# Kernel tuning notes

Hardware: AMD Instinct MI355X
Metric: run time of the kernel (lower is better)

The kernel has to match this reference:

```python
import jax, jax.numpy as jnp
import numpy as np

B, NV, NC, D, GD = 4, 2048, 8192, 64, 8


def setup_inputs() -> dict:
    key = jax.random.key(0)
    ks = jax.random.split(key, 16)
    f32 = jnp.float32
    rn = lambda k, s, fan: (jax.random.normal(k, s, dtype=f32) / np.float32(np.sqrt(fan)))
    raw = jax.random.randint(ks[0], (B, NC, NV), 0, 20)
    c_mat = jnp.where(raw == 0, -1.0, jnp.where(raw == 1, 1.0, 0.0)).astype(f32)
    v_mat = jnp.transpose(c_mat, (0, 2, 1))  # [B, NV, NC]
    variables = jax.random.normal(ks[1], (B, NV, D), dtype=f32)
    ground_vars = jax.random.normal(ks[2], (B, NV, GD), dtype=f32)
    # learned params
    c_block = rn(ks[3], (2, D, D), D)  # pos/neg literal projections (clause side)
    v_block = rn(ks[4], (2, D, D), D)  # pos/neg literal projections (variable side)
    vb = jax.random.normal(ks[5], (D,), dtype=f32)
    cb = jax.random.normal(ks[6], (D,), dtype=f32)
    Wg = rn(ks[7], (D, GD + D), GD + D)  # ground combiner Linear(concat) -> D
    bg = jnp.zeros((D,), f32)
    Wz = rn(ks[8], (D, D), D); Uz = rn(ks[9], (D, D), D); bz = jnp.zeros((D,), f32)
    Wr = rn(ks[10], (D, D), D); Ur = rn(ks[11], (D, D), D); br = jnp.zeros((D,), f32)
    Wh = rn(ks[12], (D, D), D); Uh = rn(ks[13], (D, D), D); bh = jnp.zeros((D,), f32)
    return dict(variables=variables, ground_vars=ground_vars, c_mat=c_mat, v_mat=v_mat,
                c_block=c_block, v_block=v_block, vb=vb, cb=cb, Wg=Wg, bg=bg,
                Wz=Wz, Uz=Uz, bz=bz, Wr=Wr, Ur=Ur, br=br, Wh=Wh, Uh=Uh, bh=bh)


def reference(variables, ground_vars, c_mat, v_mat, c_block, v_block, vb, cb,
              Wg, bg, Wz, Uz, bz, Wr, Ur, br, Wh, Uh, bh):
    b, nv, d = variables.shape
    v = variables.reshape(-1, d)  # [B*NV, D]
    # clause-side literal projections: bmm(c_block, v^T)^T == v @ c_block[i]^T
    pos_vars = (v @ c_block[0].T).reshape(b, nv, d)
    neg_vars = (v @ c_block[1].T).reshape(b, nv, d)
    pos_cmat = jnp.clip(c_mat, 0.0, 1.0)
    neg_cmat = -jnp.clip(c_mat, -1.0, 0.0)
    c = (jnp.einsum('bcv,bvd->bcd', pos_cmat, pos_vars)
         + jnp.einsum('bcv,bvd->bcd', neg_cmat, neg_vars))  # [B, NC, D]
    c = jax.nn.relu(c + cb)
    cv = c.reshape(-1, d)  # [B*NC, D]
    pos_cvars = (cv @ v_block[0].T).reshape(b, -1, d)
    neg_cvars = (cv @ v_block[1].T).reshape(b, -1, d)
    pos_vmat = jnp.clip(v_mat, 0.0, 1.0)
    neg_vmat = -jnp.clip(v_mat, -1.0, 0.0)
    nv_msg = (jnp.einsum('bvc,bcd->bvd', pos_vmat, pos_cvars)
              + jnp.einsum('bvc,bcd->bvd', neg_vmat, neg_cvars))  # [B, NV, D]
    v_emb = jax.nn.relu(nv_msg + vb).reshape(-1, d)
    # ground combiner: tanh(Linear(concat(ground, v_emb)))
    g = ground_vars.reshape(-1, ground_vars.shape[-1])
    av = jnp.tanh(jnp.concatenate([g, v_emb], axis=-1) @ Wg.T + bg)
    # GRU update against previous variable embeddings
    prev = v
    z = jax.nn.sigmoid(av @ Wz.T + prev @ Uz.T + bz)
    r = jax.nn.sigmoid(av @ Wr.T + prev @ Ur.T + br)
    h_tilda = jnp.tanh(av @ Wh.T + (r * prev) @ Uh.T + bh)
    h = (1.0 - z) * prev + z * h_tilda
    return h.reshape(b, nv * d, 1)
```

## Files before the change

### kernel.cpp

```cpp
#include <hip/hip_runtime.h>
#include <hip/hip_bf16.h>
#include <stdint.h>

#define NBATCH 4
#define NV 2048
#define NC 8192
#define DD 64

typedef __attribute__((ext_vector_type(8))) short s16x8;
typedef __attribute__((ext_vector_type(4))) float fx4;
typedef __attribute__((ext_vector_type(8))) unsigned short u16x8;
typedef __attribute__((ext_vector_type(4))) int i32x4;
typedef __attribute__((ext_vector_type(2))) unsigned int u32x2;

static __device__ __forceinline__ void gload_lds16(const void* g, void* l) {
    __builtin_amdgcn_global_load_lds(
        (const __attribute__((address_space(1))) unsigned int*)g,
        (__attribute__((address_space(3))) unsigned int*)l, 16, 0, 0);
}

__global__ __launch_bounds__(256) void k_prep_pv(
    const float* __restrict__ vars, const float* __restrict__ cblk,
    char* __restrict__ qsh, char* __restrict__ qsl,
    char* __restrict__ qdh, char* __restrict__ qdl)
{
    __shared__ float sv[32][64];
    __shared__ float scb[2][64][65];
    int blk = blockIdx.x;
    int b = blk >> 6, ch = blk & 63;
    int t = threadIdx.x;
    const float* vsrc = vars + ((size_t)b * NV + (size_t)ch * 32) * DD;
    for (int i = t; i < 32 * 64; i += 256) sv[i >> 6][i & 63] = vsrc[i];
    for (int i = t; i < 2 * 64 * 64; i += 256) {
        int pn = i >> 12, dout = (i >> 6) & 63, k = i & 63;
        scb[pn][k][dout] = cblk[i];
    }
    __syncthreads();
    int ks = t >> 6, dout = t & 63;
    unsigned int wsh[2] = {0, 0}, wsl[2] = {0, 0}, wdh[2] = {0, 0}, wdl[2] = {0, 0};
    #pragma unroll
    for (int c8 = 0; c8 < 8; ++c8) {
        int vloc = ks * 8 + c8;
        float ap = 0.f, an = 0.f;
        for (int k = 0; k < 64; ++k) {
            float vv = sv[vloc][k];
            ap += vv * scb[0][k][dout];
            an += vv * scb[1][k][dout];
        }
        float s = (ap + an) * 0.5f, dv = (ap - an) * 0.5f;
        int qs_ = (int)rintf(s * 4096.f);
        int qd_ = (int)rintf(dv * 4096.f);
        qs_ = min(max(qs_, -32511), 32511);
        qd_ = min(max(qd_, -32511), 32511);
        int sh = (qs_ + 128) >> 8, sl = qs_ - (sh << 8);
        int dh = (qd_ + 128) >> 8, dl = qd_ - (dh << 8);
        int w = c8 >> 2, sft = (c8 & 3) * 8;
        wsh[w] |= (unsigned int)(sh & 0xFF) << sft;
        wsl[w] |= (unsigned int)(sl & 0xFF) << sft;
        wdh[w] |= (unsigned int)(dh & 0xFF) << sft;
        wdl[w] |= (unsigned int)(dl & 0xFF) << sft;
    }
    int kc = ch >> 1;
    int lg = ((ch & 1) << 1) | (ks >> 1);
    size_t off = (((size_t)(b * 32 + kc) * 64 + dout) * 4 + lg) * 16 + (ks & 1) * 8;
    *(u32x2*)(qsh + off) = (u32x2){wsh[0], wsh[1]};
    *(u32x2*)(qsl + off) = (u32x2){wsl[0], wsl[1]};
    *(u32x2*)(qdh + off) = (u32x2){wdh[0], wdh[1]};
    *(u32x2*)(qdl + off) = (u32x2){wdl[0], wdl[1]};
}

__global__ __launch_bounds__(256) void k_compress(
    const float* __restrict__ cmat,
    char* __restrict__ asgn, unsigned short* __restrict__ comp)
{
    __shared__ char sb[64][272];
    int blk = blockIdx.x;
    int tv = blk & 7;
    int rg = (blk >> 3) & 127;
    int b = blk >> 10;
    int t = threadIdx.x;
    int wv = t >> 6, l = t & 63;
    int crow0 = rg * 64;
    const float* src = cmat + (size_t)b * NC * NV + (size_t)crow0 * NV + tv * 256;
    #pragma unroll 4
    for (int rr = 0; rr < 16; ++rr) {
        int r = wv * 16 + rr;
        fx4 x = *(const fx4*)(src + (size_t)r * NV + l * 4);
        unsigned int pk = ((unsigned int)((int)x[0] & 0xFF))
                        | (((unsigned int)((int)x[1] & 0xFF)) << 8)
                        | (((unsigned int)((int)x[2] & 0xFF)) << 16)
                        | (((unsigned int)((int)x[3] & 0xFF)) << 24);
        *(unsigned int*)&sb[r][l * 4] = pk;
    }
    __syncthreads();
    size_t abase = ((size_t)(b * 128 + tv * 16)) * 8192 * 16;
    #pragma unroll
    for (int ff = 0; ff < 4; ++ff) {
        int f = wv * 4 + ff;
        i32x4 v = *(const i32x4*)&sb[l][f * 16];
        *(i32x4*)(asgn + abase + ((size_t)f * 8192 + crow0 + l) * 16) = v;
    }
    unsigned short* cbp = comp + ((size_t)b * 256 + tv * 32) * NC + crow0;
    #pragma unroll
    for (int it = 0; it < 8; ++it) {
        int idx = it * 256 + t;
        int v8l = idx >> 6, r = idx & 63;
        const unsigned char* p = (const unsigned char*)&sb[r][v8l * 8];
        unsigned int c0 = 0;
        #pragma unroll
        for (int i = 0; i < 8; ++i) c0 |= ((unsigned int)(p[i] & 3u)) << (2 * i);
        cbp[(size_t)v8l * NC + r] = (unsigned short)c0;
    }
}

__global__ __launch_bounds__(256, 4) void k_phaseA(
    const char* __restrict__ asgn,
    const char* __restrict__ qsh, const char* __restrict__ qsl,
    const char* __restrict__ qdh, const char* __restrict__ qdl,
    float* __restrict__ cpart)
{
    __shared__ char lds[2][16384];
    int blk = blockIdx.x;
    int combo = blk & 15;
    int rg = blk >> 4;
    int b = combo >> 2;
    int q = combo & 3;
    int t = threadIdx.x;
    int wv = t >> 6, l = t & 63, lr = l & 15, lg = l >> 4;
    int c0 = rg * 128 + wv * 32;

    i32x4 ahi[2][4], alo[2][4];
    #pragma unroll
    for (int i = 0; i < 2; ++i)
        #pragma unroll
        for (int j = 0; j < 4; ++j) { ahi[i][j] = (i32x4){0,0,0,0}; alo[i][j] = (i32x4){0,0,0,0}; }

    {
        size_t gb = ((size_t)(b * 32 + q * 8)) * 4096 + (size_t)t * 16;
        char* lp = &lds[0][t * 16];
        gload_lds16(qsh + gb, lp);
        gload_lds16(qsl + gb, lp + 4096);
        gload_lds16(qdh + gb, lp + 8192);
        gload_lds16(qdl + gb, lp + 12288);
    }
    __syncthreads();

    int cur = 0;
    #pragma unroll 1
    for (int cc = 0; cc < 8; ++cc) {
        int kc = q * 8 + cc;
        if (cc < 7) {
            size_t gb = ((size_t)(b * 32 + kc + 1)) * 4096 + (size_t)t * 16;
            char* lp = &lds[cur ^ 1][t * 16];
            gload_lds16(qsh + gb, lp);
            gload_lds16(qsl + gb, lp + 4096);
            gload_lds16(qdh + gb, lp + 8192);
            gload_lds16(qdl + gb, lp + 12288);
        }
        i32x4 Asgn[2], Aabs[2];
        #pragma unroll
        for (int rt = 0; rt < 2; ++rt) {
            size_t ao = (((size_t)(b * 128 + kc * 4 + lg)) * 8192
                         + (size_t)(c0 + rt * 16 + lr)) * 16;
            i32x4 sg = *(const i32x4*)(asgn + ao);
            Asgn[rt] = sg;
            i32x4 ab;
            #pragma unroll
            for (int w = 0; w < 4; ++w) ab[w] = sg[w] & 0x01010101;
            Aabs[rt] = ab;
        }
        const char* bufp = lds[cur];
        #pragma unroll
        for (int n = 0; n < 4; ++n) {
            int boff = ((n * 16 + lr) * 4 + lg) * 16;
            i32x4 Bsh = *(const i32x4*)(bufp + boff);
            i32x4 Bsl = *(const i32x4*)(bufp + 4096 + boff);
            i32x4 Bdh = *(const i32x4*)(bufp + 8192 + boff);
            i32x4 Bdl = *(const i32x4*)(bufp + 12288 + boff);
            #pragma unroll
            for (int rt = 0; rt < 2; ++rt) {
                ahi[rt][n] = __builtin_amdgcn_mfma_i32_16x16x64_i8(Aabs[rt], Bsh, ahi[rt][n], 0, 0, 0);
                ahi[rt][n] = __builtin_amdgcn_mfma_i32_16x16x64_i8(Asgn[rt], Bdh, ahi[rt][n], 0, 0, 0);
                alo[rt][n] = __builtin_amdgcn_mfma_i32_16x16x64_i8(Aabs[rt], Bsl, alo[rt][n], 0, 0, 0);
                alo[rt][n] = __builtin_amdgcn_mfma_i32_16x16x64_i8(Asgn[rt], Bdl, alo[rt][n], 0, 0, 0);
            }
        }
        __syncthreads();
        cur ^= 1;
    }
    float* dst = cpart + (((size_t)q * NBATCH + b) * NC + c0) * DD;
    #pragma unroll
    for (int rt = 0; rt < 2; ++rt)
        #pragma unroll
        for (int n = 0; n < 4; ++n)
            #pragma unroll
            for (int r = 0; r < 4; ++r) {
                float v = (float)(ahi[rt][n][r] * 256 + alo[rt][n][r]) * (1.0f / 4096.0f);
                dst[(size_t)(rt * 16 + lg * 4 + r) * DD + n * 16 + lr] = v;
            }
}

__global__ __launch_bounds__(256) void k_projC(
    const float* __restrict__ cpart, const float* __restrict__ cb,
    const float* __restrict__ vblk,
    char* __restrict__ csh, char* __restrict__ csl,
    char* __restrict__ cdh, char* __restrict__ cdl)
{
    __shared__ float src[32][64];
    __shared__ float svb[2][64][65];
    int blk = blockIdx.x;
    int b = blk >> 8, kc32 = blk & 255;
    int t = threadIdx.x;
    const size_t qs = (size_t)NBATCH * NC * DD;
    const float* cs = cpart + ((size_t)b * NC + (size_t)kc32 * 32) * DD;
    for (int i = t; i < 2048; i += 256) {
        int k = i & 63;
        float v = cb[k];
        #pragma unroll
        for (int p = 0; p < 4; ++p) v += cs[i + p * qs];
        src[i >> 6][k] = fmaxf(v, 0.f);
    }
    for (int i = t; i < 8192; i += 256) {
        int pn = i >> 12, dout = (i >> 6) & 63, k = i & 63;
        svb[pn][k][dout] = vblk[i];
    }
    __syncthreads();
    int ks = t >> 6, dout = t & 63;
    float ap[8] = {0.f, 0.f, 0.f, 0.f, 0.f, 0.f, 0.f, 0.f};
    float an[8] = {0.f, 0.f, 0.f, 0.f, 0.f, 0.f, 0.f, 0.f};
    for (int k = 0; k < 64; ++k) {
        float w0 = svb[0][k][dout], w1 = svb[1][k][dout];
        #pragma unroll
        for (int c8 = 0; c8 < 8; ++c8) {
            float rc = src[ks * 8 + c8][k];
            ap[c8] += rc * w0;
            an[c8] += rc * w1;
        }
    }
    unsigned int wsh[2] = {0, 0}, wsl[2] = {0, 0}, wdh[2] = {0, 0}, wdl[2] = {0, 0};
    #pragma unroll
    for (int c8 = 0; c8 < 8; ++c8) {
        float s = (ap[c8] + an[c8]) * 0.5f, dv = (ap[c8] - an[c8]) * 0.5f;
        int q_s = (int)rintf(s * 512.f);
        int q_d = (int)rintf(dv * 512.f);
        q_s = min(max(q_s, -32511), 32511);
        q_d = min(max(q_d, -32511), 32511);
        int sh = (q_s + 128) >> 8, sl = q_s - (sh << 8);
        int dh = (q_d + 128) >> 8, dl = q_d - (dh << 8);
        int w = c8 >> 2, sft = (c8 & 3) * 8;
        wsh[w] |= (unsigned int)(sh & 0xFF) << sft;
        wsl[w] |= (unsigned int)(sl & 0xFF) << sft;
        wdh[w] |= (unsigned int)(dh & 0xFF) << sft;
        wdl[w] |= (unsigned int)(dl & 0xFF) << sft;
    }
    int kc = kc32 >> 1;
    int lgw = ((kc32 & 1) << 1) | (ks >> 1);
    size_t off = (((size_t)(b * 128 + kc) * 64 + dout) * 4 + lgw) * 16 + (ks & 1) * 8;
    *(u32x2*)(csh + off) = (u32x2){wsh[0], wsh[1]};
    *(u32x2*)(csl + off) = (u32x2){wsl[0], wsl[1]};
    *(u32x2*)(cdh + off) = (u32x2){wdh[0], wdh[1]};
    *(u32x2*)(cdl + off) = (u32x2){wdl[0], wdl[1]};
}

__global__ __launch_bounds__(256, 4) void k_phaseB(
    const unsigned short* __restrict__ comp,
    const char* __restrict__ csh, const char* __restrict__ csl,
    const char* __restrict__ cdh, const char* __restrict__ cdl,
    float* __restrict__ npart)
{
    __shared__ char lds[2][16384];
    int blk = blockIdx.x;
    int combo = blk & 63;
    int rg = blk >> 6;
    int b = combo >> 4;
    int q = combo & 15;
    int t = threadIdx.x;
    int wv = t >> 6, l = t & 63, lr = l & 15, lg = l >> 4;
    int v0 = rg * 128 + wv * 32;
    const unsigned short* compb = comp + (size_t)b * 256 * NC;
    int sh_ = 2 * (lr & 7);
    const unsigned short* cp0 = compb + (size_t)((v0 + lr) >> 3) * NC + q * 512 + lg * 16;
    const unsigned short* cp1 = compb + (size_t)((v0 + 16 + lr) >> 3) * NC + q * 512 + lg * 16;
    const size_t cbase = ((size_t)(b * 128 + q * 8)) * 4096;

    i32x4 ahi[2][4], alo[2][4];
    #pragma unroll
    for (int i = 0; i < 2; ++i)
        #pragma unroll
        for (int j = 0; j < 4; ++j) { ahi[i][j] = (i32x4){0,0,0,0}; alo[i][j] = (i32x4){0,0,0,0}; }

    {
        size_t gb = cbase + (size_t)t * 16;
        char* lp = &lds[0][t * 16];
        gload_lds16(csh + gb, lp);
        gload_lds16(csl + gb, lp + 4096);
        gload_lds16(cdh + gb, lp + 8192);
        gload_lds16(cdl + gb, lp + 12288);
    }
    __syncthreads();

    int cur = 0;
    #pragma unroll 1
    for (int cc = 0; cc < 8; ++cc) {
        u16x8 u00 = *(const u16x8*)(cp0 + cc * 64);
        u16x8 u01 = *(const u16x8*)(cp0 + cc * 64 + 8);
        u16x8 u10 = *(const u16x8*)(cp1 + cc * 64);
        u16x8 u11 = *(const u16x8*)(cp1 + cc * 64 + 8);
        if (cc < 7) {
            size_t gb = cbase + (size_t)(cc + 1) * 4096 + (size_t)t * 16;
            char* lp = &lds[cur ^ 1][t * 16];
            gload_lds16(csh + gb, lp);
            gload_lds16(csl + gb, lp + 4096);
            gload_lds16(cdh + gb, lp + 8192);
            gload_lds16(cdl + gb, lp + 12288);
        }
        i32x4 Asgn[2], Aabs[2];
        #pragma unroll
        for (int rt = 0; rt < 2; ++rt) {
            u16x8 ua = rt ? u10 : u00;
            u16x8 ub = rt ? u11 : u01;
            i32x4 sg;
            #pragma unroll
            for (int g = 0; g < 4; ++g) {
                unsigned int wg = 0;
                #pragma unroll
                for (int jj = 0; jj < 4; ++jj) {
                    int j = g * 4 + jj;
                    unsigned int code = ((unsigned int)(j < 8 ? ua[j & 7] : ub[j & 7]) >> sh_) & 3u;
                    unsigned int byt = (code == 3u) ? 0xFFu : code;
                    wg |= byt << (jj * 8);
                }
                sg[g] = (int)wg;
            }
            Asgn[rt] = sg;
            i32x4 ab;
            #pragma unroll
            for (int g = 0; g < 4; ++g) ab[g] = sg[g] & 0x01010101;
            Aabs[rt] = ab;
        }
        const char* bufp = lds[cur];
        #pragma unroll
        for (int n = 0; n < 4; ++n) {
            int boff = ((n * 16 + lr) * 4 + lg) * 16;
            i32x4 Bsh = *(const i32x4*)(bufp + boff);
            i32x4 Bsl = *(const i32x4*)(bufp + 4096 + boff);
            i32x4 Bdh = *(const i32x4*)(bufp + 8192 + boff);
            i32x4 Bdl = *(const i32x4*)(bufp + 12288 + boff);
            #pragma unroll
            for (int rt = 0; rt < 2; ++rt) {
                ahi[rt][n] = __builtin_amdgcn_mfma_i32_16x16x64_i8(Aabs[rt], Bsh, ahi[rt][n], 0, 0, 0);
                ahi[rt][n] = __builtin_amdgcn_mfma_i32_16x16x64_i8(Asgn[rt], Bdh, ahi[rt][n], 0, 0, 0);
                alo[rt][n] = __builtin_amdgcn_mfma_i32_16x16x64_i8(Aabs[rt], Bsl, alo[rt][n], 0, 0, 0);
                alo[rt][n] = __builtin_amdgcn_mfma_i32_16x16x64_i8(Asgn[rt], Bdl, alo[rt][n], 0, 0, 0);
            }
        }
        __syncthreads();
        cur ^= 1;
    }
    float* dst = npart + (((size_t)q * NBATCH + b) * NV + v0) * DD;
    #pragma unroll
    for (int rt = 0; rt < 2; ++rt)
        #pragma unroll
        for (int n = 0; n < 4; ++n)
            #pragma unroll
            for (int r = 0; r < 4; ++r) {
                float v = (float)(ahi[rt][n][r] * 256 + alo[rt][n][r]) * (1.0f / 512.0f);
                dst[(size_t)(rt * 16 + lg * 4 + r) * DD + n * 16 + lr] = v;
            }
}

__global__ __launch_bounds__(512) void k_gru(
    const float* __restrict__ npart, const float* __restrict__ vars,
    const float* __restrict__ gv, const float* __restrict__ vb,
    const float* __restrict__ Wg, const float* __restrict__ bg,
    const float* __restrict__ Wz, const float* __restrict__ Uz, const float* __restrict__ bz,
    const float* __restrict__ Wr, const float* __restrict__ Ur, const float* __restrict__ brr,
    const float* __restrict__ Wh, const float* __restrict__ Uh, const float* __restrict__ bh,
    float* __restrict__ out)
{
    __shared__ float sWg[72][65];
    __shared__ float sWz[64][65], sUz[64][65];
    __shared__ float sWr[64][65], sUr[64][65];
    __shared__ float sWh[64][65], sUh[64][65];
    __shared__ float scat[8][72];
    __shared__ float sprev[8][64];
    __shared__ float sav[8][64];
    __shared__ float srp[8][64];
    int t = threadIdx.x;
    for (int i = t * 4; i < 4608; i += 2048) {
        fx4 g4 = *(const fx4*)(Wg + i);
        int dout = i / 72, j = i - dout * 72;
        #pragma unroll
        for (int jj = 0; jj < 4; ++jj) sWg[j + jj][dout] = g4[jj];
    }
    for (int i = t * 4; i < 4096; i += 2048) {
        int dout = i >> 6, k = i & 63;
        fx4 a;
        a = *(const fx4*)(Wz + i);
        #pragma unroll
        for (int jj = 0; jj < 4; ++jj) sWz[k + jj][dout] = a[jj];
        a = *(const fx4*)(Uz + i);
        #pragma unroll
        for (int jj = 0; jj < 4; ++jj) sUz[k + jj][dout] = a[jj];
        a = *(const fx4*)(Wr + i);
        #pragma unroll
        for (int jj = 0; jj < 4; ++jj) sWr[k + jj][dout] = a[jj];
        a = *(const fx4*)(Ur + i);
        #pragma unroll
        for (int jj = 0; jj < 4; ++jj) sUr[k + jj][dout] = a[jj];
        a = *(const fx4*)(Wh + i);
        #pragma unroll
        for (int jj = 0; jj < 4; ++jj) sWh[k + jj][dout] = a[jj];
        a = *(const fx4*)(Uh + i);
        #pragma unroll
        for (int jj = 0; jj < 4; ++jj) sUh[k + jj][dout] = a[jj];
    }
    int rr = t >> 6, dout = t & 63;
    const size_t qs = (size_t)NBATCH * NV * DD;
    #pragma unroll 1
    for (int it = 0; it < 4; ++it) {
        size_t row = (size_t)blockIdx.x * 32 + it * 8 + rr;
        float prev = vars[row * 64 + dout];
        float ve = vb[dout];
        #pragma unroll
        for (int s = 0; s < 16; ++s) ve += npart[(size_t)s * qs + row * 64 + dout];
        ve = fmaxf(ve, 0.f);
        scat[rr][8 + dout] = ve;
        if (dout < 8) scat[rr][dout] = gv[row * 8 + dout];
        sprev[rr][dout] = prev;
        __syncthreads();
        float a = bg[dout];
        for (int j = 0; j < 72; ++j) a += scat[rr][j] * sWg[j][dout];
        float av = 1.f - 2.f / (__expf(2.f * a) + 1.f);
        sav[rr][dout] = av;
        __syncthreads();
        float zi = bz[dout], ri = brr[dout], hwa = 0.f;
        for (int k = 0; k < 64; ++k) {
            float ak = sav[rr][k], pk = sprev[rr][k];
            zi += ak * sWz[k][dout] + pk * sUz[k][dout];
            ri += ak * sWr[k][dout] + pk * sUr[k][dout];
            hwa += ak * sWh[k][dout];
        }
        float z = 1.f / (1.f + __expf(-zi));
        float rgate = 1.f / (1.f + __expf(-ri));
        srp[rr][dout] = rgate * prev;
        __syncthreads();
        float hin = bh[dout] + hwa;
        for (int k = 0; k < 64; ++k) hin += srp[rr][k] * sUh[k][dout];
        float ht = 1.f - 2.f / (__expf(2.f * hin) + 1.f);
        out[row * 64 + dout] = (1.f - z) * prev + z * ht;
        __syncthreads();
    }
}

extern "C" void kernel_launch(void* const* d_in, const int* in_sizes, int n_in,
                              void* d_out, int out_size, void* d_ws, size_t ws_size,
                              hipStream_t stream) {
    (void)in_sizes; (void)n_in; (void)out_size; (void)ws_size;
    const float* vars = (const float*)d_in[0];
    const float* gv   = (const float*)d_in[1];
    const float* cmat = (const float*)d_in[2];
    const float* cblk = (const float*)d_in[4];
    const float* vblk = (const float*)d_in[5];
    const float* vb   = (const float*)d_in[6];
    const float* cb   = (const float*)d_in[7];
    const float* Wg   = (const float*)d_in[8];
    const float* bg   = (const float*)d_in[9];
    const float* Wz   = (const float*)d_in[10];
    const float* Uz   = (const float*)d_in[11];
    const float* bz   = (const float*)d_in[12];
    const float* Wr   = (const float*)d_in[13];
    const float* Ur   = (const float*)d_in[14];
    const float* br_  = (const float*)d_in[15];
    const float* Wh   = (const float*)d_in[16];
    const float* Uh   = (const float*)d_in[17];
    const float* bh   = (const float*)d_in[18];
    float* out = (float*)d_out;

    char* w = (char*)d_ws;
    const size_t MB = 1024 * 1024;
    char* qsh = w + 0 * MB;
    char* qsl = w + 1 * MB;
    char* qdh = w + 2 * MB;
    char* qdl = w + 3 * MB;
    char* csh = w + 4 * MB;
    char* csl = w + 6 * MB;
    char* cdh = w + 8 * MB;
    char* cdl = w + 10 * MB;
    float* cpart         = (float*)(w + 12 * MB);
    float* npart         = (float*)(w + 44 * MB);
    unsigned short* comp = (unsigned short*)(w + 76 * MB);
    char* asgn           = w + 92 * MB;

    k_prep_pv<<<256, 256, 0, stream>>>(vars, cblk, qsh, qsl, qdh, qdl);
    k_compress<<<4096, 256, 0, stream>>>(cmat, asgn, comp);
    k_phaseA<<<1024, 256, 0, stream>>>(asgn, qsh, qsl, qdh, qdl, cpart);
    k_projC<<<1024, 256, 0, stream>>>(cpart, cb, vblk, csh, csl, cdh, cdl);
    k_phaseB<<<1024, 256, 0, stream>>>(comp, csh, csl, cdh, cdl, npart);
    k_gru<<<256, 512, 0, stream>>>(npart, vars, gv, vb, Wg, bg,
                                   Wz, Uz, bz, Wr, Ur, br_, Wh, Uh, bh, out);
}
```

Measured before the change: 186.3 us.

## Drop int8 sign matrix; decode 2-bit compressed adjacency inside phaseA

The compress kernel no longer writes a separate int8 signed adjacency array (64 MB total). Phase A instead reads the existing 2-bit packed `comp` array and expands it to int8 MFMA operands in registers, prefetching the next chunk's words one iteration ahead. This removes a large global write and read in exchange for extra ALU bit-unpacking in the MFMA loop and narrow 16-bit strided loads. The compress kernel also reads LDS with word loads instead of byte loads and shrinks its padding.

New measurement: 164.3 us. -11.8%, faster.

```diff
diff --git a/kernel.cpp b/kernel.cpp
--- a/kernel.cpp
+++ b/kernel.cpp
@@ -70,10 +70,9 @@
 }
 
 __global__ __launch_bounds__(256) void k_compress(
-    const float* __restrict__ cmat,
-    char* __restrict__ asgn, unsigned short* __restrict__ comp)
+    const float* __restrict__ cmat, unsigned short* __restrict__ comp)
 {
-    __shared__ char sb[64][272];
+    __shared__ char sb[64][260];
     int blk = blockIdx.x;
     int tv = blk & 7;
     int rg = (blk >> 3) & 127;
@@ -93,28 +92,24 @@
         *(unsigned int*)&sb[r][l * 4] = pk;
     }
     __syncthreads();
-    size_t abase = ((size_t)(b * 128 + tv * 16)) * 8192 * 16;
-    #pragma unroll
-    for (int ff = 0; ff < 4; ++ff) {
-        int f = wv * 4 + ff;
-        i32x4 v = *(const i32x4*)&sb[l][f * 16];
-        *(i32x4*)(asgn + abase + ((size_t)f * 8192 + crow0 + l) * 16) = v;
-    }
     unsigned short* cbp = comp + ((size_t)b * 256 + tv * 32) * NC + crow0;
     #pragma unroll
     for (int it = 0; it < 8; ++it) {
         int idx = it * 256 + t;
         int v8l = idx >> 6, r = idx & 63;
-        const unsigned char* p = (const unsigned char*)&sb[r][v8l * 8];
+        unsigned int lo = *(const unsigned int*)&sb[r][v8l * 8];
+        unsigned int hi = *(const unsigned int*)&sb[r][v8l * 8 + 4];
         unsigned int c0 = 0;
         #pragma unroll
-        for (int i = 0; i < 8; ++i) c0 |= ((unsigned int)(p[i] & 3u)) << (2 * i);
+        for (int i = 0; i < 4; ++i) c0 |= ((lo >> (8 * i)) & 3u) << (2 * i);
+        #pragma unroll
+        for (int i = 0; i < 4; ++i) c0 |= ((hi >> (8 * i)) & 3u) << (8 + 2 * i);
         cbp[(size_t)v8l * NC + r] = (unsigned short)c0;
     }
 }
 
 __global__ __launch_bounds__(256, 4) void k_phaseA(
-    const char* __restrict__ asgn,
+    const unsigned short* __restrict__ comp,
     const char* __restrict__ qsh, const char* __restrict__ qsl,
     const char* __restrict__ qdh, const char* __restrict__ qdl,
     float* __restrict__ cpart)
@@ -128,6 +123,7 @@
     int t = threadIdx.x;
     int wv = t >> 6, l = t & 63, lr = l & 15, lg = l >> 4;
     int c0 = rg * 128 + wv * 32;
+    const unsigned short* compb = comp + (size_t)b * 256 * NC;
 
     i32x4 ahi[2][4], alo[2][4];
     #pragma unroll
@@ -143,26 +139,50 @@
         gload_lds16(qdh + gb, lp + 8192);
         gload_lds16(qdl + gb, lp + 12288);
     }
+    unsigned int u0[2], u1[2], u0n[2], u1n[2];
+    #pragma unroll
+    for (int rt = 0; rt < 2; ++rt) {
+        int crow = c0 + rt * 16 + lr;
+        size_t v8 = (size_t)(q * 64 + lg * 2);
+        u0[rt] = compb[v8 * NC + crow];
+        u1[rt] = compb[(v8 + 1) * NC + crow];
+    }
     __syncthreads();
 
     int cur = 0;
     #pragma unroll 1
     for (int cc = 0; cc < 8; ++cc) {
-        int kc = q * 8 + cc;
         if (cc < 7) {
-            size_t gb = ((size_t)(b * 32 + kc + 1)) * 4096 + (size_t)t * 16;
+            size_t gb = ((size_t)(b * 32 + q * 8 + cc + 1)) * 4096 + (size_t)t * 16;
             char* lp = &lds[cur ^ 1][t * 16];
             gload_lds16(qsh + gb, lp);
             gload_lds16(qsl + gb, lp + 4096);
             gload_lds16(qdh + gb, lp + 8192);
             gload_lds16(qdl + gb, lp + 12288);
+            #pragma unroll
+            for (int rt = 0; rt < 2; ++rt) {
+                int crow = c0 + rt * 16 + lr;
+                size_t v8 = (size_t)(q * 64 + (cc + 1) * 8 + lg * 2);
+                u0n[rt] = compb[v8 * NC + crow];
+                u1n[rt] = compb[(v8 + 1) * NC + crow];
+            }
         }
         i32x4 Asgn[2], Aabs[2];
         #pragma unroll
         for (int rt = 0; rt < 2; ++rt) {
-            size_t ao = (((size_t)(b * 128 + kc * 4 + lg)) * 8192
-                         + (size_t)(c0 + rt * 16 + lr)) * 16;
-            i32x4 sg = *(const i32x4*)(asgn + ao);
+            i32x4 sg;
+            #pragma unroll
+            for (int w = 0; w < 4; ++w) {
+                unsigned int wg = 0;
+                #pragma unroll
+                for (int jj = 0; jj < 4; ++jj) {
+                    int j = w * 4 + jj;
+                    unsigned int u = (j < 8) ? u0[rt] : u1[rt];
+                    int c = ((int)(u << (30 - 2 * (j & 7)))) >> 30;
+                    wg |= ((unsigned int)c & 0xFFu) << (8 * jj);
+                }
+                sg[w] = (int)wg;
+            }
             Asgn[rt] = sg;
             i32x4 ab;
             #pragma unroll
@@ -184,6 +204,10 @@
                 alo[rt][n] = __builtin_amdgcn_mfma_i32_16x16x64_i8(Aabs[rt], Bsl, alo[rt][n], 0, 0, 0);
                 alo[rt][n] = __builtin_amdgcn_mfma_i32_16x16x64_i8(Asgn[rt], Bdl, alo[rt][n], 0, 0, 0);
             }
+        }
+        if (cc < 7) {
+            #pragma unroll
+            for (int rt = 0; rt < 2; ++rt) { u0[rt] = u0n[rt]; u1[rt] = u1n[rt]; }
         }
         __syncthreads();
         cur ^= 1;
@@ -490,11 +514,10 @@
     float* cpart         = (float*)(w + 12 * MB);
     float* npart         = (float*)(w + 44 * MB);
     unsigned short* comp = (unsigned short*)(w + 76 * MB);
-    char* asgn           = w + 92 * MB;
 
     k_prep_pv<<<256, 256, 0, stream>>>(vars, cblk, qsh, qsl, qdh, qdl);
-    k_compress<<<4096, 256, 0, stream>>>(cmat, asgn, comp);
-    k_phaseA<<<1024, 256, 0, stream>>>(asgn, qsh, qsl, qdh, qdl, cpart);
+    k_compress<<<4096, 256, 0, stream>>>(cmat, comp);
+    k_phaseA<<<1024, 256, 0, stream>>>(comp, qsh, qsl, qdh, qdl, cpart);
     k_projC<<<1024, 256, 0, stream>>>(cpart, cb, vblk, csh, csl, cdh, cdl);
     k_phaseB<<<1024, 256, 0, stream>>>(comp, csh, csl, cdh, cdl, npart);
     k_gru<<<256, 512, 0, stream>>>(npart, vars, gv, vb, Wg, bg,
```

## Fuse prep/compress kernels, fuse projC into phaseA, drop asgn and cpart buffers

Applied to the files above, without the earlier changes.

Merges the variable projection and adjacency compression into one launch, and removes the separate int8 sign buffer: phaseA now decodes its A operand from the 2-bit compressed matrix, the same way phaseB already does. phaseA no longer splits K into four partial sums. Each block accumulates all 32 K chunks for 64 clause rows and then applies bias, ReLU and the v_block projection in-kernel. This eliminates the float cpart round trip through global memory and one launch. In exchange phaseA runs only 512 blocks with a longer serial K loop and lower occupancy (launch bounds 2), so latency hiding may suffer.

New measurement: 152.2 us, median of 3. -18.3%, faster.

```diff
diff --git a/kernel.cpp b/kernel.cpp
--- a/kernel.cpp
+++ b/kernel.cpp
@@ -19,157 +19,159 @@
         (__attribute__((address_space(3))) unsigned int*)l, 16, 0, 0);
 }
 
-__global__ __launch_bounds__(256) void k_prep_pv(
+__global__ __launch_bounds__(256) void k_front(
+    const float* __restrict__ cmat, unsigned short* __restrict__ comp,
     const float* __restrict__ vars, const float* __restrict__ cblk,
     char* __restrict__ qsh, char* __restrict__ qsl,
     char* __restrict__ qdh, char* __restrict__ qdl)
 {
-    __shared__ float sv[32][64];
-    __shared__ float scb[2][64][65];
+    __shared__ __align__(16) char pool[41472];
     int blk = blockIdx.x;
-    int b = blk >> 6, ch = blk & 63;
     int t = threadIdx.x;
-    const float* vsrc = vars + ((size_t)b * NV + (size_t)ch * 32) * DD;
-    for (int i = t; i < 32 * 64; i += 256) sv[i >> 6][i & 63] = vsrc[i];
-    for (int i = t; i < 2 * 64 * 64; i += 256) {
-        int pn = i >> 12, dout = (i >> 6) & 63, k = i & 63;
-        scb[pn][k][dout] = cblk[i];
-    }
-    __syncthreads();
-    int ks = t >> 6, dout = t & 63;
-    unsigned int wsh[2] = {0, 0}, wsl[2] = {0, 0}, wdh[2] = {0, 0}, wdl[2] = {0, 0};
-    #pragma unroll
-    for (int c8 = 0; c8 < 8; ++c8) {
-        int vloc = ks * 8 + c8;
-        float ap = 0.f, an = 0.f;
-        for (int k = 0; k < 64; ++k) {
-            float vv = sv[vloc][k];
-            ap += vv * scb[0][k][dout];
-            an += vv * scb[1][k][dout];
-        }
-        float s = (ap + an) * 0.5f, dv = (ap - an) * 0.5f;
-        int qs_ = (int)rintf(s * 4096.f);
-        int qd_ = (int)rintf(dv * 4096.f);
-        qs_ = min(max(qs_, -32511), 32511);
-        qd_ = min(max(qd_, -32511), 32511);
-        int sh = (qs_ + 128) >> 8, sl = qs_ - (sh << 8);
-        int dh = (qd_ + 128) >> 8, dl = qd_ - (dh << 8);
-        int w = c8 >> 2, sft = (c8 & 3) * 8;
-        wsh[w] |= (unsigned int)(sh & 0xFF) << sft;
-        wsl[w] |= (unsigned int)(sl & 0xFF) << sft;
-        wdh[w] |= (unsigned int)(dh & 0xFF) << sft;
-        wdl[w] |= (unsigned int)(dl & 0xFF) << sft;
-    }
-    int kc = ch >> 1;
-    int lg = ((ch & 1) << 1) | (ks >> 1);
-    size_t off = (((size_t)(b * 32 + kc) * 64 + dout) * 4 + lg) * 16 + (ks & 1) * 8;
-    *(u32x2*)(qsh + off) = (u32x2){wsh[0], wsh[1]};
-    *(u32x2*)(qsl + off) = (u32x2){wsl[0], wsl[1]};
-    *(u32x2*)(qdh + off) = (u32x2){wdh[0], wdh[1]};
-    *(u32x2*)(qdl + off) = (u32x2){wdl[0], wdl[1]};
-}
-
-__global__ __launch_bounds__(256) void k_compress(
-    const float* __restrict__ cmat,
-    char* __restrict__ asgn, unsigned short* __restrict__ comp)
-{
-    __shared__ char sb[64][272];
-    int blk = blockIdx.x;
-    int tv = blk & 7;
-    int rg = (blk >> 3) & 127;
-    int b = blk >> 10;
-    int t = threadIdx.x;
-    int wv = t >> 6, l = t & 63;
-    int crow0 = rg * 64;
-    const float* src = cmat + (size_t)b * NC * NV + (size_t)crow0 * NV + tv * 256;
-    #pragma unroll 4
-    for (int rr = 0; rr < 16; ++rr) {
-        int r = wv * 16 + rr;
-        fx4 x = *(const fx4*)(src + (size_t)r * NV + l * 4);
-        unsigned int pk = ((unsigned int)((int)x[0] & 0xFF))
-                        | (((unsigned int)((int)x[1] & 0xFF)) << 8)
-                        | (((unsigned int)((int)x[2] & 0xFF)) << 16)
-                        | (((unsigned int)((int)x[3] & 0xFF)) << 24);
-        *(unsigned int*)&sb[r][l * 4] = pk;
-    }
-    __syncthreads();
-    size_t abase = ((size_t)(b * 128 + tv * 16)) * 8192 * 16;
-    #pragma unroll
-    for (int ff = 0; ff < 4; ++ff) {
-        int f = wv * 4 + ff;
-        i32x4 v = *(const i32x4*)&sb[l][f * 16];
-        *(i32x4*)(asgn + abase + ((size_t)f * 8192 + crow0 + l) * 16) = v;
-    }
-    unsigned short* cbp = comp + ((size_t)b * 256 + tv * 32) * NC + crow0;
-    #pragma unroll
-    for (int it = 0; it < 8; ++it) {
-        int idx = it * 256 + t;
-        int v8l = idx >> 6, r = idx & 63;
-        const unsigned char* p = (const unsigned char*)&sb[r][v8l * 8];
-        unsigned int c0 = 0;
-        #pragma unroll
-        for (int i = 0; i < 8; ++i) c0 |= ((unsigned int)(p[i] & 3u)) << (2 * i);
-        cbp[(size_t)v8l * NC + r] = (unsigned short)c0;
-    }
-}
-
-__global__ __launch_bounds__(256, 4) void k_phaseA(
-    const char* __restrict__ asgn,
+    if (blk < 4096) {
+        char (*sb)[260] = (char(*)[260])pool;
+        int tv = blk & 7;
+        int rg = (blk >> 3) & 127;
+        int b = blk >> 10;
+        int wv = t >> 6, l = t & 63;
+        int crow0 = rg * 64;
+        const float* src = cmat + (size_t)b * NC * NV + (size_t)crow0 * NV + tv * 256;
+        #pragma unroll 4
+        for (int rr = 0; rr < 16; ++rr) {
+            int r = wv * 16 + rr;
+            fx4 x = *(const fx4*)(src + (size_t)r * NV + l * 4);
+            unsigned int pk = ((unsigned int)((int)x[0] & 0xFF))
+                            | (((unsigned int)((int)x[1] & 0xFF)) << 8)
+                            | (((unsigned int)((int)x[2] & 0xFF)) << 16)
+                            | (((unsigned int)((int)x[3] & 0xFF)) << 24);
+            *(unsigned int*)&sb[r][l * 4] = pk;
+        }
+        __syncthreads();
+        unsigned short* cbp = comp + ((size_t)b * 256 + tv * 32) * NC + crow0;
+        #pragma unroll
+        for (int it = 0; it < 8; ++it) {
+            int idx = it * 256 + t;
+            int v8l = idx >> 6, r = idx & 63;
+            unsigned int lo = *(const unsigned int*)&sb[r][v8l * 8];
+            unsigned int hi = *(const unsigned int*)&sb[r][v8l * 8 + 4];
+            unsigned int c0 = 0;
+            #pragma unroll
+            for (int i = 0; i < 4; ++i) c0 |= ((lo >> (8 * i)) & 3u) << (2 * i);
+            #pragma unroll
+            for (int i = 0; i < 4; ++i) c0 |= ((hi >> (8 * i)) & 3u) << (8 + 2 * i);
+            cbp[(size_t)v8l * NC + r] = (unsigned short)c0;
+        }
+    } else {
+        float (*sv)[64] = (float(*)[64])pool;
+        float (*scb)[65] = (float(*)[65])(pool + 8192);
+        int blk2 = blk - 4096;
+        int b = blk2 >> 6, ch = blk2 & 63;
+        const float* vsrc = vars + ((size_t)b * NV + (size_t)ch * 32) * DD;
+        for (int i = t; i < 32 * 64; i += 256) sv[i >> 6][i & 63] = vsrc[i];
+        for (int i = t; i < 2 * 64 * 64; i += 256) {
+            int pn = i >> 12, dout = (i >> 6) & 63, k = i & 63;
+            scb[pn * 64 + k][dout] = cblk[i];
+        }
+        __syncthreads();
+        int ks = t >> 6, dout = t & 63;
+        unsigned int wsh[2] = {0, 0}, wsl[2] = {0, 0}, wdh[2] = {0, 0}, wdl[2] = {0, 0};
+        #pragma unroll
+        for (int c8 = 0; c8 < 8; ++c8) {
+            int vloc = ks * 8 + c8;
+            float ap = 0.f, an = 0.f;
+            for (int k = 0; k < 64; ++k) {
+                float vv = sv[vloc][k];
+                ap += vv * scb[k][dout];
+                an += vv * scb[64 + k][dout];
+            }
+            float s = (ap + an) * 0.5f, dv = (ap - an) * 0.5f;
+            int qs_ = (int)rintf(s * 4096.f);
+            int qd_ = (int)rintf(dv * 4096.f);
+            qs_ = min(max(qs_, -32511), 32511);
+            qd_ = min(max(qd_, -32511), 32511);
+            int sh = (qs_ + 128) >> 8, sl = qs_ - (sh << 8);
+            int dh = (qd_ + 128) >> 8, dl = qd_ - (dh << 8);
+            int w = c8 >> 2, sft = (c8 & 3) * 8;
+            wsh[w] |= (unsigned int)(sh & 0xFF) << sft;
+            wsl[w] |= (unsigned int)(sl & 0xFF) << sft;
+            wdh[w] |= (unsigned int)(dh & 0xFF) << sft;
+            wdl[w] |= (unsigned int)(dl & 0xFF) << sft;
+        }
+        int kc = ch >> 1;
+        int lg = ((ch & 1) << 1) | (ks >> 1);
+        size_t off = (((size_t)(b * 32 + kc) * 64 + dout) * 4 + lg) * 16 + (ks & 1) * 8;
+        *(u32x2*)(qsh + off) = (u32x2){wsh[0], wsh[1]};
+        *(u32x2*)(qsl + off) = (u32x2){wsl[0], wsl[1]};
+        *(u32x2*)(qdh + off) = (u32x2){wdh[0], wdh[1]};
+        *(u32x2*)(qdl + off) = (u32x2){wdl[0], wdl[1]};
+    }
+}
+
+__global__ __launch_bounds__(256, 2) void k_phaseA(
+    const unsigned short* __restrict__ comp,
     const char* __restrict__ qsh, const char* __restrict__ qsl,
     const char* __restrict__ qdh, const char* __restrict__ qdl,
-    float* __restrict__ cpart)
+    const float* __restrict__ cb, const float* __restrict__ vblk,
+    char* __restrict__ csh, char* __restrict__ csl,
+    char* __restrict__ cdh, char* __restrict__ cdl)
 {
-    __shared__ char lds[2][16384];
+    __shared__ __align__(16) char pool[50176];
     int blk = blockIdx.x;
-    int combo = blk & 15;
-    int rg = blk >> 4;
-    int b = combo >> 2;
-    int q = combo & 3;
+    int b = blk & 3;
+    int rg = blk >> 2;
     int t = threadIdx.x;
     int wv = t >> 6, l = t & 63, lr = l & 15, lg = l >> 4;
-    int c0 = rg * 128 + wv * 32;
-
-    i32x4 ahi[2][4], alo[2][4];
-    #pragma unroll
-    for (int i = 0; i < 2; ++i)
-        #pragma unroll
-        for (int j = 0; j < 4; ++j) { ahi[i][j] = (i32x4){0,0,0,0}; alo[i][j] = (i32x4){0,0,0,0}; }
+    int crow0 = rg * 64;
+    int crow = crow0 + wv * 16 + lr;
+    const unsigned short* compb = comp + (size_t)b * 256 * NC;
+
+    i32x4 ahi[4], alo[4];
+    #pragma unroll
+    for (int n = 0; n < 4; ++n) { ahi[n] = (i32x4){0,0,0,0}; alo[n] = (i32x4){0,0,0,0}; }
 
     {
-        size_t gb = ((size_t)(b * 32 + q * 8)) * 4096 + (size_t)t * 16;
-        char* lp = &lds[0][t * 16];
+        size_t gb = ((size_t)(b * 32)) * 4096 + (size_t)t * 16;
+        char* lp = pool + t * 16;
         gload_lds16(qsh + gb, lp);
         gload_lds16(qsl + gb, lp + 4096);
         gload_lds16(qdh + gb, lp + 8192);
         gload_lds16(qdl + gb, lp + 12288);
     }
+    unsigned int u0, u1, u0n, u1n;
+    u0 = compb[(size_t)(lg * 2) * NC + crow];
+    u1 = compb[(size_t)(lg * 2 + 1) * NC + crow];
     __syncthreads();
 
     int cur = 0;
     #pragma unroll 1
-    for (int cc = 0; cc < 8; ++cc) {
-        int kc = q * 8 + cc;
-        if (cc < 7) {
+    for (int kc = 0; kc < 32; ++kc) {
+        if (kc < 31) {
             size_t gb = ((size_t)(b * 32 + kc + 1)) * 4096 + (size_t)t * 16;
-            char* lp = &lds[cur ^ 1][t * 16];
+            char* lp = pool + (cur ^ 1) * 16384 + t * 16;
             gload_lds16(qsh + gb, lp);
             gload_lds16(qsl + gb, lp + 4096);
             gload_lds16(qdh + gb, lp + 8192);
             gload_lds16(qdl + gb, lp + 12288);
-        }
-        i32x4 Asgn[2], Aabs[2];
-        #pragma unroll
-        for (int rt = 0; rt < 2; ++rt) {
-            size_t ao = (((size_t)(b * 128 + kc * 4 + lg)) * 8192
-                         + (size_t)(c0 + rt * 16 + lr)) * 16;
-            i32x4 sg = *(const i32x4*)(asgn + ao);
-            Asgn[rt] = sg;
-            i32x4 ab;
-            #pragma unroll
-            for (int w = 0; w < 4; ++w) ab[w] = sg[w] & 0x01010101;
-            Aabs[rt] = ab;
-        }
-        const char* bufp = lds[cur];
+            size_t v8 = (size_t)((kc + 1) * 8 + lg * 2);
+            u0n = compb[v8 * NC + crow];
+            u1n = compb[(v8 + 1) * NC + crow];
+        }
+        i32x4 Asgn, Aabs;
+        #pragma unroll
+        for (int w = 0; w < 4; ++w) {
+            unsigned int wg = 0;
+            #pragma unroll
+            for (int jj = 0; jj < 4; ++jj) {
+                int j = w * 4 + jj;
+                unsigned int u = (j < 8) ? u0 : u1;
+                int c = ((int)(u << (30 - 2 * (j & 7)))) >> 30;
+                wg |= ((unsigned int)c & 0xFFu) << (8 * jj);
+            }
+            Asgn[w] = (int)wg;
+        }
+        #pragma unroll
+        for (int w = 0; w < 4; ++w) Aabs[w] = Asgn[w] & 0x01010101;
+        const char* bufp = pool + cur * 16384;
         #pragma unroll
         for (int n = 0; n < 4; ++n) {
             int boff = ((n * 16 + lr) * 4 + lg) * 16;
@@ -177,69 +179,54 @@
             i32x4 Bsl = *(const i32x4*)(bufp + 4096 + boff);
             i32x4 Bdh = *(const i32x4*)(bufp + 8192 + boff);
             i32x4 Bdl = *(const i32x4*)(bufp + 12288 + boff);
-            #pragma unroll
-            for (int rt = 0; rt < 2; ++rt) {
-                ahi[rt][n] = __builtin_amdgcn_mfma_i32_16x16x64_i8(Aabs[rt], Bsh, ahi[rt][n], 0, 0, 0);
-                ahi[rt][n] = __builtin_amdgcn_mfma_i32_16x16x64_i8(Asgn[rt], Bdh, ahi[rt][n], 0, 0, 0);
-                alo[rt][n] = __builtin_amdgcn_mfma_i32_16x16x64_i8(Aabs[rt], Bsl, alo[rt][n], 0, 0, 0);
-                alo[rt][n] = __builtin_amdgcn_mfma_i32_16x16x64_i8(Asgn[rt], Bdl, alo[rt][n], 0, 0, 0);
-            }
-        }
+            ahi[n] = __builtin_amdgcn_mfma_i32_16x16x64_i8(Aabs, Bsh, ahi[n], 0, 0, 0);
+            ahi[n] = __builtin_amdgcn_mfma_i32_16x16x64_i8(Asgn, Bdh, ahi[n], 0, 0, 0);
+            alo[n] = __builtin_amdgcn_mfma_i32_16x16x64_i8(Aabs, Bsl, alo[n], 0, 0, 0);
+            alo[n] = __builtin_amdgcn_mfma_i32_16x16x64_i8(Asgn, Bdl, alo[n], 0, 0, 0);
+        }
+        if (kc < 31) { u0 = u0n; u1 = u1n; }
         __syncthreads();
         cur ^= 1;
     }
-    float* dst = cpart + (((size_t)q * NBATCH + b) * NC + c0) * DD;
-    #pragma unroll
-    for (int rt = 0; rt < 2; ++rt)
-        #pragma unroll
-        for (int n = 0; n < 4; ++n)
-            #pragma unroll
-            for (int r = 0; r < 4; ++r) {
-                float v = (float)(ahi[rt][n][r] * 256 + alo[rt][n][r]) * (1.0f / 4096.0f);
-                dst[(size_t)(rt * 16 + lg * 4 + r) * DD + n * 16 + lr] = v;
-            }
-}
-
-__global__ __launch_bounds__(256) void k_projC(
-    const float* __restrict__ cpart, const float* __restrict__ cb,
-    const float* __restrict__ vblk,
-    char* __restrict__ csh, char* __restrict__ csl,
-    char* __restrict__ cdh, char* __restrict__ cdl)
-{
-    __shared__ float src[32][64];
-    __shared__ float svb[2][64][65];
-    int blk = blockIdx.x;
-    int b = blk >> 8, kc32 = blk & 255;
-    int t = threadIdx.x;
-    const size_t qs = (size_t)NBATCH * NC * DD;
-    const float* cs = cpart + ((size_t)b * NC + (size_t)kc32 * 32) * DD;
-    for (int i = t; i < 2048; i += 256) {
-        int k = i & 63;
-        float v = cb[k];
-        #pragma unroll
-        for (int p = 0; p < 4; ++p) v += cs[i + p * qs];
-        src[i >> 6][k] = fmaxf(v, 0.f);
-    }
-    for (int i = t; i < 8192; i += 256) {
-        int pn = i >> 12, dout = (i >> 6) & 63, k = i & 63;
-        svb[pn][k][dout] = vblk[i];
+
+    int* sbC = (int*)pool;
+    float* sbCf = (float*)pool;
+    float* svb = (float*)(pool + 64 * 66 * 4);
+    #pragma unroll
+    for (int n = 0; n < 4; ++n)
+        #pragma unroll
+        for (int r = 0; r < 4; ++r)
+            sbC[(wv * 16 + lg * 4 + r) * 66 + n * 16 + lr] = ahi[n][r] * 256 + alo[n][r];
+    for (int i = t * 4; i < 8192; i += 1024) {
+        fx4 g4 = *(const fx4*)(vblk + i);
+        int pn = i >> 12, dout = (i >> 6) & 63, k0 = i & 63;
+        #pragma unroll
+        for (int jj = 0; jj < 4; ++jj) svb[(pn * 64 + k0 + jj) * 65 + dout] = g4[jj];
     }
     __syncthreads();
-    int ks = t >> 6, dout = t & 63;
-    float ap[8] = {0.f, 0.f, 0.f, 0.f, 0.f, 0.f, 0.f, 0.f};
-    float an[8] = {0.f, 0.f, 0.f, 0.f, 0.f, 0.f, 0.f, 0.f};
+    for (int idx = t; idx < 4096; idx += 256) {
+        int row = idx >> 6, k = idx & 63;
+        float f = (float)sbC[row * 66 + k] * (1.0f / 4096.0f) + cb[k];
+        sbCf[row * 66 + k] = fmaxf(f, 0.f);
+    }
+    __syncthreads();
+    int dout = l;
+    float ap[16], an[16];
+    #pragma unroll
+    for (int c8 = 0; c8 < 16; ++c8) { ap[c8] = 0.f; an[c8] = 0.f; }
     for (int k = 0; k < 64; ++k) {
-        float w0 = svb[0][k][dout], w1 = svb[1][k][dout];
-        #pragma unroll
-        for (int c8 = 0; c8 < 8; ++c8) {
-            float rc = src[ks * 8 + c8][k];
+        float w0 = svb[k * 65 + dout];
+        float w1 = svb[(64 + k) * 65 + dout];
+        #pragma unroll
+        for (int c8 = 0; c8 < 16; ++c8) {
+            float rc = sbCf[(wv * 16 + c8) * 66 + k];
             ap[c8] += rc * w0;
             an[c8] += rc * w1;
         }
     }
-    unsigned int wsh[2] = {0, 0}, wsl[2] = {0, 0}, wdh[2] = {0, 0}, wdl[2] = {0, 0};
-    #pragma unroll
-    for (int c8 = 0; c8 < 8; ++c8) {
+    unsigned int osh[4] = {0,0,0,0}, osl[4] = {0,0,0,0}, odh[4] = {0,0,0,0}, odl[4] = {0,0,0,0};
+    #pragma unroll
+    for (int c8 = 0; c8 < 16; ++c8) {
         float s = (ap[c8] + an[c8]) * 0.5f, dv = (ap[c8] - an[c8]) * 0.5f;
         int q_s = (int)rintf(s * 512.f);
         int q_d = (int)rintf(dv * 512.f);
@@ -248,18 +235,16 @@
         int sh = (q_s + 128) >> 8, sl = q_s - (sh << 8);
         int dh = (q_d + 128) >> 8, dl = q_d - (dh << 8);
         int w = c8 >> 2, sft = (c8 & 3) * 8;
-        wsh[w] |= (unsigned int)(sh & 0xFF) << sft;
-        wsl[w] |= (unsigned int)(sl & 0xFF) << sft;
-        wdh[w] |= (unsigned int)(dh & 0xFF) << sft;
-        wdl[w] |= (unsigned int)(dl & 0xFF) << sft;
-    }
-    int kc = kc32 >> 1;
-    int lgw = ((kc32 & 1) << 1) | (ks >> 1);
-    size_t off = (((size_t)(b * 128 + kc) * 64 + dout) * 4 + lgw) * 16 + (ks & 1) * 8;
-    *(u32x2*)(csh + off) = (u32x2){wsh[0], wsh[1]};
-    *(u32x2*)(csl + off) = (u32x2){wsl[0], wsl[1]};
-    *(u32x2*)(cdh + off) = (u32x2){wdh[0], wdh[1]};
-    *(u32x2*)(cdl + off) = (u32x2){wdl[0], wdl[1]};
+        osh[w] |= (unsigned int)(sh & 0xFF) << sft;
+        osl[w] |= (unsigned int)(sl & 0xFF) << sft;
+        odh[w] |= (unsigned int)(dh & 0xFF) << sft;
+        odl[w] |= (unsigned int)(dl & 0xFF) << sft;
+    }
+    size_t off = (((size_t)(b * 128 + rg) * 64 + dout) * 64) + wv * 16;
+    *(i32x4*)(csh + off) = (i32x4){(int)osh[0], (int)osh[1], (int)osh[2], (int)osh[3]};
+    *(i32x4*)(csl + off) = (i32x4){(int)osl[0], (int)osl[1], (int)osl[2], (int)osl[3]};
+    *(i32x4*)(cdh + off) = (i32x4){(int)odh[0], (int)odh[1], (int)odh[2], (int)odh[3]};
+    *(i32x4*)(cdl + off) = (i32x4){(int)odl[0], (int)odl[1], (int)odl[2], (int)odl[3]};
 }
 
 __global__ __launch_bounds__(256, 4) void k_phaseB(
@@ -338,7 +323,7 @@
             for (int g = 0; g < 4; ++g) ab[g] = sg[g] & 0x01010101;
             Aabs[rt] = ab;
         }
-        const char* bufp = lds[cur];
+        const char* bufp = &lds[cur][0];
         #pragma unroll
         for (int n = 0; n < 4; ++n) {
             int boff = ((n * 16 + lr) * 4 + lg) * 16;
@@ -487,15 +472,12 @@
     char* csl = w + 6 * MB;
     char* cdh = w + 8 * MB;
     char* cdl = w + 10 * MB;
-    float* cpart         = (float*)(w + 12 * MB);
-    float* npart         = (float*)(w + 44 * MB);
-    unsigned short* comp = (unsigned short*)(w + 76 * MB);
-    char* asgn           = w + 92 * MB;
-
-    k_prep_pv<<<256, 256, 0, stream>>>(vars, cblk, qsh, qsl, qdh, qdl);
-    k_compress<<<4096, 256, 0, stream>>>(cmat, asgn, comp);
-    k_phaseA<<<1024, 256, 0, stream>>>(asgn, qsh, qsl, qdh, qdl, cpart);
-    k_projC<<<1024, 256, 0, stream>>>(cpart, cb, vblk, csh, csl, cdh, cdl);
+    float* npart         = (float*)(w + 12 * MB);
+    unsigned short* comp = (unsigned short*)(w + 44 * MB);
+
+    k_front<<<4352, 256, 0, stream>>>(cmat, comp, vars, cblk, qsh, qsl, qdh, qdl);
+    k_phaseA<<<512, 256, 0, stream>>>(comp, qsh, qsl, qdh, qdl, cb, vblk,
+                                      csh, csl, cdh, cdl);
     k_phaseB<<<1024, 256, 0, stream>>>(comp, csh, csl, cdh, cdl, npart);
     k_gru<<<256, 512, 0, stream>>>(npart, vars, gv, vb, Wg, bg,
                                    Wz, Uz, bz, Wr, Ur, br_, Wh, Uh, bh, out);
```
